# Kernel optimization log

Hardware: AMD Instinct MI355X
Metric: run time of the kernel (lower is better)

The kernel has to match this reference:

```python
import jax, jax.numpy as jnp
import numpy as np

NUM_HEADS = 128
QK_NOPE = 128
QK_ROPE = 64
V_HEAD = 128
Q_HEAD_DIM = 192
SOFTMAX_SCALE = 1.0 / np.sqrt(192.0)


def _rope_interleave(x, cos, sin):
    # x: [b,h,s,d]; reorder interleaved pairs to half-split layout then rotate
    b, h, s, d = x.shape
    x = x.reshape(b, h, s, d // 2, 2).swapaxes(3, 4).reshape(b, h, s, d)
    x1, x2 = x[..., : d // 2], x[..., d // 2:]
    rot = jnp.concatenate([-x2, x1], axis=-1)
    return x * cos + rot * sin


def setup_inputs() -> dict:
    key = jax.random.key(0)
    ks = jax.random.split(key, 8)
    bsz, q_len = 16, 1
    q_lora, kv_lora = 1536, 512
    cache_cap = 4096
    start_pos = 2048
    s = 0.05
    q_normed_dn = jax.random.normal(ks[0], (bsz, q_len, q_lora), jnp.float32) * s
    compressed_kv = jax.random.normal(ks[1], (bsz, q_len, kv_lora), jnp.float32) * s
    k_pe = jax.random.normal(ks[2], (bsz, 1, q_len, QK_ROPE), jnp.float32) * s
    position_ids = jnp.full((bsz, q_len), start_pos, dtype=jnp.int64)
    ckv_cache = jax.random.normal(ks[3], (bsz, cache_cap, kv_lora), jnp.float32) * s
    k_pe_cache = jax.random.normal(ks[4], (bsz, cache_cap, QK_ROPE), jnp.float32) * s
    # rope caches over full positions
    pos = jnp.arange(cache_cap, dtype=jnp.float32)
    inv = 1.0 / (10000.0 ** (jnp.arange(0, QK_ROPE, 2, dtype=jnp.float32) / QK_ROPE))
    freqs = pos[:, None] * inv[None, :]
    emb = jnp.concatenate([freqs, freqs], axis=-1)
    sin_cache = jnp.sin(emb)
    cos_cache = jnp.cos(emb)
    wkv_b = jax.random.normal(ks[5], (NUM_HEADS, QK_NOPE + V_HEAD, kv_lora), jnp.float32) * s
    wq_b = jax.random.normal(ks[6], (NUM_HEADS * Q_HEAD_DIM, q_lora), jnp.float32) * s
    return {
        "q_normed_dn": q_normed_dn,
        "compressed_kv": compressed_kv,
        "k_pe": k_pe,
        "position_ids": position_ids,
        "start_pos": start_pos,
        "ckv_cache": ckv_cache,
        "k_pe_cache": k_pe_cache,
        "sin_cache": sin_cache,
        "cos_cache": cos_cache,
        "wkv_b": wkv_b,
        "wq_b": wq_b,
    }


def reference(q_normed_dn, compressed_kv, k_pe, position_ids, start_pos,
              ckv_cache, k_pe_cache, sin_cache, cos_cache, wkv_b, wq_b):
    bsz, q_len, q_lora = q_normed_dn.shape
    kv_lora = compressed_kv.shape[-1]

    # split absorbed query projection
    wq_b_t = wq_b.T.reshape(q_lora, NUM_HEADS, Q_HEAD_DIM)  # [l,h,192]
    q_nope = jnp.einsum('bsl,lhd->bhsd', q_normed_dn, wq_b_t[:, :, :QK_NOPE])
    q_pe = jnp.einsum('bsl,lhd->bhsd', q_normed_dn, wq_b_t[:, :, QK_NOPE:])

    # matrix absorption: q_nope projected into latent space via w_ukv
    w_ukv = wkv_b[:, :QK_NOPE]                         # [h,128,c]
    q_nope = jnp.einsum('bshd,hdc->bshc', q_nope.swapaxes(1, 2), w_ukv)  # [b,s,h,c]

    # RoPE on q_pe and k_pe using gathered cos/sin at position_ids
    cos = cos_cache[position_ids][:, None]   # [b,1,s,d]
    sin = sin_cache[position_ids][:, None]
    q_pe = _rope_interleave(q_pe, cos, sin)            # [b,h,s,64]
    k_pe = _rope_interleave(k_pe, cos, sin)            # [b,1,s,64]
    q_pe = q_pe.swapaxes(1, 2)                         # [b,s,h,64]
    k_pe = k_pe[:, 0]                                  # [b,s,64]

    # append new tokens to caches at start_pos (q_len new tokens)
    ckv_cache = jax.lax.dynamic_update_slice(ckv_cache, compressed_kv, (0, start_pos, 0))
    k_pe_cache = jax.lax.dynamic_update_slice(k_pe_cache, k_pe, (0, start_pos, 0))
    kv_len = start_pos + q_len
    ckv = ckv_cache[:, :kv_len]                        # [b,n,c]
    kpe = k_pe_cache[:, :kv_len]                       # [b,n,64]

    # MLA decode attention in latent space (q_len==1, causal trivially satisfied)
    # scores = q_nope . ckv + q_pe . kpe
    scores = (jnp.einsum('bshc,bnc->bhsn', q_nope, ckv) +
              jnp.einsum('bshd,bnd->bhsn', q_pe, kpe)) * SOFTMAX_SCALE
    probs = jax.nn.softmax(scores, axis=-1)
    o = jnp.einsum('bhsn,bnc->bshc', probs, ckv)       # [b,s,h,c]
    o = o.reshape(bsz * q_len, NUM_HEADS, kv_lora)

    # project latent output to v_head_dim via tail of wkv_b
    attn_output = jnp.einsum('bhc,hdc->bhd', o, wkv_b[:, -V_HEAD:])
    return attn_output
```

## Files before the change

kernel.cpp:

```cpp
#include <hip/hip_runtime.h>
#include <hip/hip_bf16.h>
#include <math.h>

typedef __attribute__((ext_vector_type(8))) short short8x;
typedef __attribute__((ext_vector_type(4))) float f32x4;
typedef __attribute__((ext_vector_type(4))) unsigned short u16x4;
typedef __attribute__((ext_vector_type(8))) unsigned short u16x8;

#define NSPLIT 16
#define NTILE 66
#define KVROWS (NTILE * 32)

__device__ __forceinline__ unsigned short f2bf(float x) {
  unsigned int u = __float_as_uint(x);
  u += 0x7fffu + ((u >> 16) & 1u);
  return (unsigned short)(u >> 16);
}
__device__ __forceinline__ float bf2f(unsigned short u) {
  return __uint_as_float(((unsigned int)u) << 16);
}
__device__ __forceinline__ u16x4 cvt4(float4 v) {
  u16x4 r;
  r[0] = f2bf(v.x); r[1] = f2bf(v.y); r[2] = f2bf(v.z); r[3] = f2bf(v.w);
  return r;
}
__device__ __forceinline__ void gload_lds16(const void* g, void* l) {
  __builtin_amdgcn_global_load_lds(
      (const __attribute__((address_space(1))) unsigned int*)g,
      (__attribute__((address_space(3))) unsigned int*)l, 16, 0, 0);
}

__global__ __launch_bounds__(256) void kA(
    const float* __restrict__ ckvc, const float* __restrict__ kpec,
    const float* __restrict__ ckvn, const float* __restrict__ kpein,
    const float* __restrict__ cosc, const float* __restrict__ sinc,
    const int* __restrict__ sposp, int cap,
    unsigned short* __restrict__ kvbf,
    const float* __restrict__ wq, const float* __restrict__ x,
    float* __restrict__ qfull) {
  const int bx = blockIdx.x;
  const int tid = threadIdx.x;

  if (bx < 384) {
    const int lane = tid & 63, wid = tid >> 6;
    const int l15 = lane & 15, lg = lane >> 4;
    const int rowb = bx * 64 + wid * 16;
    const float* wrow = wq + (size_t)(rowb + l15) * 1536 + lg * 8;
    const float* xrow = x + l15 * 1536 + lg * 8;

    f32x4 aHH = (f32x4){0.f, 0.f, 0.f, 0.f};
    f32x4 aHL = (f32x4){0.f, 0.f, 0.f, 0.f};
    f32x4 aLH = (f32x4){0.f, 0.f, 0.f, 0.f};
    f32x4 bHH = (f32x4){0.f, 0.f, 0.f, 0.f};
    f32x4 bHL = (f32x4){0.f, 0.f, 0.f, 0.f};
    f32x4 bLH = (f32x4){0.f, 0.f, 0.f, 0.f};
#pragma unroll 8
    for (int kc = 0; kc < 48; ++kc) {
      const float4 wA = *(const float4*)(wrow + kc * 32);
      const float4 wB = *(const float4*)(wrow + kc * 32 + 4);
      const float4 xA = *(const float4*)(xrow + kc * 32);
      const float4 xB = *(const float4*)(xrow + kc * 32 + 4);
      const float wf[8] = {wA.x, wA.y, wA.z, wA.w, wB.x, wB.y, wB.z, wB.w};
      const float xf[8] = {xA.x, xA.y, xA.z, xA.w, xB.x, xB.y, xB.z, xB.w};
      short8x ah, al, bh, bl;
#pragma unroll
      for (int e = 0; e < 8; ++e) {
        const unsigned int wu = __float_as_uint(wf[e]);
        const float whf = __uint_as_float(wu & 0xffff0000u);
        ah[e] = (short)(wu >> 16);
        al[e] = (short)(__float_as_uint(wf[e] - whf) >> 16);
        const unsigned int xu = __float_as_uint(xf[e]);
        const float xhf = __uint_as_float(xu & 0xffff0000u);
        bh[e] = (short)(xu >> 16);
        bl[e] = (short)(__float_as_uint(xf[e] - xhf) >> 16);
      }
      if (kc & 1) {
        bHH = __builtin_amdgcn_mfma_f32_16x16x32_bf16(ah, bh, bHH, 0, 0, 0);
        bHL = __builtin_amdgcn_mfma_f32_16x16x32_bf16(ah, bl, bHL, 0, 0, 0);
        bLH = __builtin_amdgcn_mfma_f32_16x16x32_bf16(al, bh, bLH, 0, 0, 0);
      } else {
        aHH = __builtin_amdgcn_mfma_f32_16x16x32_bf16(ah, bh, aHH, 0, 0, 0);
        aHL = __builtin_amdgcn_mfma_f32_16x16x32_bf16(ah, bl, aHL, 0, 0, 0);
        aLH = __builtin_amdgcn_mfma_f32_16x16x32_bf16(al, bh, aLH, 0, 0, 0);
      }
    }
    const f32x4 acc = (aHH + bHH) + (aHL + bHL) + (aLH + bLH);
#pragma unroll
    for (int r = 0; r < 4; ++r)
      qfull[(size_t)l15 * 24576 + rowb + lg * 4 + r] = acc[r];
  } else {
    const int bxx = bx - 384;
    const int spos = sposp[0];
#pragma unroll
    for (int i = 0; i < 8; ++i) {
      const int u = bxx * 2048 + i * 256 + tid;
      const int b = u / 304128;
      const int r = u - b * 304128;
      const int n = r / 144;
      const int c4 = (r - n * 144) * 4;
      float4 v = make_float4(0.f, 0.f, 0.f, 0.f);
      if (n < spos) {
        if (c4 < 512) v = *(const float4*)(ckvc + ((size_t)b * cap + n) * 512 + c4);
        else          v = *(const float4*)(kpec + ((size_t)b * cap + n) * 64 + (c4 - 512));
      } else if (n == spos) {
        if (c4 < 512) v = *(const float4*)(ckvn + (size_t)b * 512 + c4);
        else {
          const int d = c4 - 512;
          const float* kp = kpein + b * 64;
          float o[4];
          if (d < 32) {
#pragma unroll
            for (int k = 0; k < 4; ++k) {
              int j = d + k;
              o[k] = kp[2 * j] * cosc[spos * 64 + j] - kp[2 * j + 1] * sinc[spos * 64 + j];
            }
          } else {
#pragma unroll
            for (int k = 0; k < 4; ++k) {
              int j = d - 32 + k;
              o[k] = kp[2 * j + 1] * cosc[spos * 64 + j] + kp[2 * j] * sinc[spos * 64 + j];
            }
          }
          v = make_float4(o[0], o[1], o[2], o[3]);
        }
      }
      *(u16x4*)(kvbf + (size_t)u * 4) = cvt4(v);
    }
  }
}

__global__ __launch_bounds__(256) void kB2(
    const float* __restrict__ qfull, const float* __restrict__ wkv,
    const float* __restrict__ cosc, const float* __restrict__ sinc,
    const int* __restrict__ sposp, unsigned short* __restrict__ qcat,
    const unsigned short* __restrict__ kvbf, unsigned short* __restrict__ vT) {
  __shared__ __align__(16) unsigned char shbuf[36864];
  const int bx = blockIdx.x;
  const int tid = threadIdx.x;

  if (bx < 256) {
    float* qs = (float*)shbuf;
    const int h = bx & 127;
    const int half = bx >> 7;
    for (int u = tid; u < 2048; u += 256) {
      int bb = u >> 7, d = u & 127;
      qs[u] = qfull[bb * 24576 + h * 192 + d];
    }
    __syncthreads();
    const int c = half * 256 + tid;
    float acc[16];
#pragma unroll
    for (int bb = 0; bb < 16; ++bb) acc[bb] = 0.f;
    const float* wbase = wkv + (size_t)h * 256 * 512;
    for (int d = 0; d < 128; ++d) {
      const float w = wbase[d * 512 + c];
#pragma unroll
      for (int bb = 0; bb < 16; ++bb) acc[bb] += qs[bb * 128 + d] * w;
    }
#pragma unroll
    for (int bb = 0; bb < 16; ++bb)
      qcat[(size_t)(bb * 128 + h) * 576 + c] = f2bf(acc[bb]);
  } else if (bx < 272) {
    const int b = bx - 256;
    const int pos = sposp[0];
#pragma unroll
    for (int i = 0; i < 16; ++i) {
      int idx = tid + i * 256;
      int h = idx >> 5, j = idx & 31;
      const float cj = cosc[pos * 64 + j];
      const float sj = sinc[pos * 64 + j];
      const float* src = qfull + b * 24576 + h * 192 + 128;
      float x0 = src[2 * j], x1 = src[2 * j + 1];
      unsigned short* dst = qcat + (size_t)(b * 128 + h) * 576 + 512;
      dst[j] = f2bf(x0 * cj - x1 * sj);
      dst[j + 32] = f2bf(x1 * cj + x0 * sj);
    }
  } else {
    unsigned short* tile_sh = (unsigned short*)shbuf;
    const int v_ = bx - 272;
    const int b = v_ / NTILE;
    const int tile = v_ - b * NTILE;
    const int wid = tid >> 6;
    const unsigned short* src = kvbf + ((size_t)b * KVROWS + tile * 32) * 576;
#pragma unroll
    for (int i = 0; i < 9; ++i) {
      const int ch = i * 256 + tid;
      const int row = ch / 72, cc = ch - row * 72;
      gload_lds16(src + row * 576 + ((cc ^ (row & 7)) * 8),
                  &tile_sh[(i * 256 + wid * 64) * 8]);
    }
    __syncthreads();
    unsigned short* vdst = vT + ((size_t)b * NTILE + tile) * 18432;
#pragma unroll
    for (int r = 0; r < 9; ++r) {
      const int c = r * 64 + (tid >> 2);
      const int q = tid & 3;
      const int c8 = c >> 3, c7 = c & 7;
      u16x8 w;
#pragma unroll
      for (int j = 0; j < 8; ++j)
        w[j] = tile_sh[(q * 8 + j) * 576 + ((c8 ^ j) << 3) + c7];
      *(u16x8*)(vdst + c * 32 + q * 8) = w;
    }
  }
}

__global__ __launch_bounds__(512, 2) void k4_attn(
    const unsigned short* __restrict__ kvbf, const unsigned short* __restrict__ vT,
    const unsigned short* __restrict__ qcat, const int* __restrict__ sposp,
    unsigned short* __restrict__ opart, float* __restrict__ mlp) {
  __shared__ __align__(16) unsigned short kv_sh[2][32 * 576];
  __shared__ __align__(16) unsigned short vt_sh[2][512 * 32];
  __shared__ __align__(16) unsigned short p_sh[8 * 640];

  const int tid = threadIdx.x;
  const int split = blockIdx.x, b = blockIdx.y;
  const int kvlen = sposp[0] + 1;
  const int lane = tid & 63, wid = tid >> 6;
  const int l15 = lane & 15, lg = lane >> 4;

  const unsigned short* kvb = kvbf + (size_t)b * KVROWS * 576;
  const unsigned short* vtb = vT + (size_t)b * NTILE * 18432;

  const int vro = lane >> 2, vq = lane & 3;
  const int vgq = vq ^ ((vro >> 1) & 3);

  auto STAGE = [&](int pb, int tt) {
    const unsigned short* ksrc = kvb + (size_t)tt * 32 * 576;
    for (int j = wid; j < 36; j += 8) {
      int u = j * 64 + lane;
      int row = u / 72, cc = u - row * 72;
      gload_lds16(ksrc + row * 576 + ((cc ^ (row & 7)) * 8), &kv_sh[pb][j * 512]);
    }
    const unsigned short* vsrc = vtb + (size_t)tt * 18432;
    for (int j = wid; j < 32; j += 8)
      gload_lds16(vsrc + j * 512 + vro * 32 + vgq * 8, &vt_sh[pb][j * 512]);
  };

  STAGE(0, split);

  const int hrow = b * 128 + wid * 16 + l15;
  const unsigned short* qrow = qcat + (size_t)hrow * 576;
  short8x qf[18];
#pragma unroll
  for (int s = 0; s < 18; ++s)
    qf[s] = *(const short8x*)(qrow + s * 32 + lg * 8);

  f32x4 acc[32];
#pragma unroll
  for (int i = 0; i < 32; ++i) acc[i] = (f32x4){0.f, 0.f, 0.f, 0.f};
  float mold[4] = {-1e30f, -1e30f, -1e30f, -1e30f};
  float lsum[4] = {0.f, 0.f, 0.f, 0.f};
  const float C2 = (1.0f / sqrtf(192.0f)) * 1.4426950408889634f;

  const int vrd = ((lg ^ ((l15 >> 1) & 3)) << 3);

  int pb = 0;
  for (int tt = split; tt * 32 < kvlen; tt += NSPLIT, pb ^= 1) {
    __syncthreads();
    if ((tt + NSPLIT) * 32 < kvlen) STAGE(pb ^ 1, tt + NSPLIT);
    const int n0 = tt * 32;

    f32x4 D0 = (f32x4){0.f, 0.f, 0.f, 0.f};
    f32x4 D1 = (f32x4){0.f, 0.f, 0.f, 0.f};
#pragma unroll
    for (int s = 0; s < 18; ++s) {
      const int c8 = (s * 4 + lg) ^ (l15 & 7);
      short8x fb0 = *(const short8x*)&kv_sh[pb][l15 * 576 + c8 * 8];
      short8x fb1 = *(const short8x*)&kv_sh[pb][(16 + l15) * 576 + c8 * 8];
      D0 = __builtin_amdgcn_mfma_f32_16x16x32_bf16(qf[s], fb0, D0, 0, 0, 0);
      D1 = __builtin_amdgcn_mfma_f32_16x16x32_bf16(qf[s], fb1, D1, 0, 0, 0);
    }

    const bool v0 = (n0 + l15) < kvlen;
    const bool v1 = (n0 + 16 + l15) < kvlen;
    float alpha[4];
#pragma unroll
    for (int r = 0; r < 4; ++r) {
      const float t0 = v0 ? D0[r] * C2 : -1e30f;
      const float t1 = v1 ? D1[r] * C2 : -1e30f;
      float mx = fmaxf(t0, t1);
      mx = fmaxf(mx, __shfl_xor(mx, 1, 64));
      mx = fmaxf(mx, __shfl_xor(mx, 2, 64));
      mx = fmaxf(mx, __shfl_xor(mx, 4, 64));
      mx = fmaxf(mx, __shfl_xor(mx, 8, 64));
      const float mn = fmaxf(mold[r], mx);
      alpha[r] = exp2f(mold[r] - mn);
      const float p0 = v0 ? exp2f(t0 - mn) : 0.f;
      const float p1 = v1 ? exp2f(t1 - mn) : 0.f;
      float rs = p0 + p1;
      rs += __shfl_xor(rs, 1, 64);
      rs += __shfl_xor(rs, 2, 64);
      rs += __shfl_xor(rs, 4, 64);
      rs += __shfl_xor(rs, 8, 64);
      lsum[r] = lsum[r] * alpha[r] + rs;
      mold[r] = mn;
      p_sh[wid * 640 + (lg * 4 + r) * 40 + l15] = f2bf(p0);
      p_sh[wid * 640 + (lg * 4 + r) * 40 + 16 + l15] = f2bf(p1);
    }
    const f32x4 av = {alpha[0], alpha[1], alpha[2], alpha[3]};
#pragma unroll
    for (int cg = 0; cg < 32; ++cg) acc[cg] *= av;

    const short8x pa = *(const short8x*)&p_sh[wid * 640 + l15 * 40 + lg * 8];
#pragma unroll
    for (int cg = 0; cg < 32; ++cg) {
      short8x bv = *(const short8x*)&vt_sh[pb][cg * 512 + l15 * 32 + vrd];
      acc[cg] = __builtin_amdgcn_mfma_f32_16x16x32_bf16(pa, bv, acc[cg], 0, 0, 0);
    }
  }

  const int hbm_ = b * 128 + wid * 16 + lg * 4;
  if (l15 == 0) {
#pragma unroll
    for (int r = 0; r < 4; ++r) {
      mlp[(size_t)(hbm_ + r) * (2 * NSPLIT) + split * 2] = mold[r];
      mlp[(size_t)(hbm_ + r) * (2 * NSPLIT) + split * 2 + 1] = lsum[r];
    }
  }

  __syncthreads();
  unsigned short* ep = &kv_sh[0][0] + wid * 8192;
#pragma unroll
  for (int cg = 0; cg < 32; ++cg)
#pragma unroll
    for (int r = 0; r < 4; ++r)
      ep[(lg * 4 + r) * 512 + cg * 16 + l15] = f2bf(acc[cg][r]);
#pragma unroll
  for (int r16 = 0; r16 < 16; ++r16) {
    const int bh = b * 128 + wid * 16 + r16;
    const size_t ob = ((size_t)bh * NSPLIT + split) * 512;
#pragma unroll
    for (int i = 0; i < 2; ++i)
      *(u16x4*)&opart[ob + i * 256 + lane * 4] =
          *(const u16x4*)&ep[r16 * 512 + i * 256 + lane * 4];
  }
}

__global__ __launch_bounds__(512) void kC_out(
    const unsigned short* __restrict__ opart, const float* __restrict__ mlp,
    const float* __restrict__ wkv, float* __restrict__ out) {
  __shared__ float os[16 * 512];
  __shared__ float wsc[16 * 16];
  __shared__ float lsc[16];
  const int h = blockIdx.x;
  const int tid = threadIdx.x;

  if (tid < 16) {
    const int b = tid;
    const float* m = mlp + (size_t)(b * 128 + h) * (2 * NSPLIT);
    float mi[NSPLIT], li[NSPLIT], M = -1e30f;
#pragma unroll
    for (int i = 0; i < NSPLIT; ++i) {
      mi[i] = m[i * 2];
      li[i] = m[i * 2 + 1];
      M = fmaxf(M, mi[i]);
    }
    float Ls = 0.f;
#pragma unroll
    for (int i = 0; i < NSPLIT; ++i) {
      const float w = exp2f(mi[i] - M);
      Ls += li[i] * w;
      wsc[b * NSPLIT + i] = w;
    }
    lsc[b] = Ls;
  }
  __syncthreads();

  for (int u = tid; u < 8192; u += 512) {
    const int b = u >> 9, c = u & 511;
    const unsigned short* op = opart + (size_t)(b * 128 + h) * NSPLIT * 512 + c;
    float o = 0.f;
#pragma unroll
    for (int i = 0; i < NSPLIT; ++i) o += wsc[b * NSPLIT + i] * bf2f(op[i * 512]);
    os[u] = o / lsc[b];
  }
  __syncthreads();

  const int d = tid >> 2, cq = tid & 3;
  const float* wrow = wkv + ((size_t)(h * 256 + 128 + d)) * 512;
  float acc[16];
#pragma unroll
  for (int bb = 0; bb < 16; ++bb) acc[bb] = 0.f;
  for (int i = 0; i < 32; ++i) {
    const int c = cq * 4 + i * 16;
    const float4 w4 = *(const float4*)&wrow[c];
#pragma unroll
    for (int bb = 0; bb < 16; ++bb) {
      const float4 o4 = *(const float4*)&os[bb * 512 + c];
      acc[bb] += w4.x * o4.x + w4.y * o4.y + w4.z * o4.z + w4.w * o4.w;
    }
  }
#pragma unroll
  for (int bb = 0; bb < 16; ++bb) {
    float v = acc[bb];
    v += __shfl_xor(v, 1, 64);
    v += __shfl_xor(v, 2, 64);
    if (cq == 0) out[(size_t)(bb * 128 + h) * 128 + d] = v;
  }
}

extern "C" void kernel_launch(void* const* d_in, const int* in_sizes, int n_in,
                              void* d_out, int out_size, void* d_ws, size_t ws_size,
                              hipStream_t stream) {
  const float* x = (const float*)d_in[0];
  const float* ckvn = (const float*)d_in[1];
  const float* kpein = (const float*)d_in[2];
  const int* sposp = (const int*)d_in[4];
  const float* ckvc = (const float*)d_in[5];
  const float* kpec = (const float*)d_in[6];
  const float* sinc = (const float*)d_in[7];
  const float* cosc = (const float*)d_in[8];
  const float* wkv = (const float*)d_in[9];
  const float* wq = (const float*)d_in[10];
  float* out = (float*)d_out;

  const int cap = in_sizes[5] / (16 * 512);

  float* ws = (float*)d_ws;
  float* qfull = ws;
  float* mlp = ws + 393216;
  unsigned short* qcat = (unsigned short*)(ws + 458752);
  unsigned short* kvbf = (unsigned short*)(ws + 1048576);
  unsigned short* vT   = (unsigned short*)(ws + 10780672);
  unsigned short* opart = (unsigned short*)(ws + 20512768);

  kA<<<dim3(384 + 2376), 256, 0, stream>>>(ckvc, kpec, ckvn, kpein, cosc, sinc,
                                           sposp, cap, kvbf, wq, x, qfull);
  kB2<<<dim3(272 + NTILE * 16), 256, 0, stream>>>(qfull, wkv, cosc, sinc, sposp,
                                                  qcat, kvbf, vT);
  k4_attn<<<dim3(NSPLIT, 16), 512, 0, stream>>>(kvbf, vT, qcat, sposp, opart, mlp);
  kC_out<<<dim3(128), 512, 0, stream>>>(opart, mlp, wkv, out);
}
```

Measured before the change: 177.2 us.

## Split q-projection into separate LDS-staged split-K GEMM kernel with more blocks

Separates the fused kernel into two launches: a cache-packing kernel that converts the KV cache to bf16, and a new q-projection GEMM kernel. The new GEMM stages 8 weight rows per block into swizzled LDS via direct global-to-LDS loads. It splits the K dimension across the 4 waves and reduces the partial sums through LDS, which lifts the grid from 384 to 3072 blocks. The aim is better bandwidth and occupancy on the large wq read, at the cost of an extra kernel launch, wasted MFMA columns (only 8 of 16 rows are used), and losing the overlap that came from running both tasks in one launch.

```diff
diff --git a/kernel.cpp b/kernel.cpp
--- a/kernel.cpp
+++ b/kernel.cpp
@@ -30,102 +30,127 @@
       (__attribute__((address_space(3))) unsigned int*)l, 16, 0, 0);
 }
 
-__global__ __launch_bounds__(256) void kA(
+__global__ __launch_bounds__(256, 3) void k1q(
+    const float* __restrict__ wq, const float* __restrict__ x,
+    float* __restrict__ qfull) {
+  __shared__ __align__(16) float wlds[8 * 1536];
+  const int bx = blockIdx.x;
+  const int tid = threadIdx.x;
+  const int lane = tid & 63, wid = tid >> 6;
+  const int l15 = lane & 15, lg = lane >> 4;
+
+  const float* wqb = wq + (size_t)bx * 8 * 1536;
+#pragma unroll
+  for (int i = 0; i < 12; ++i) {
+    const int u = i * 256 + tid;
+    const int row = u / 384;
+    const int cw = u - row * 384;
+    gload_lds16(wqb + ((size_t)row * 384 + (cw ^ (row & 7))) * 4, &wlds[u * 4]);
+  }
+
+  const int arow = l15 & 7;
+  const float* xrow = x + (size_t)l15 * 1536 + wid * 384 + lg * 8;
+
+  f32x4 aHH = (f32x4){0.f, 0.f, 0.f, 0.f};
+  f32x4 aHL = (f32x4){0.f, 0.f, 0.f, 0.f};
+  f32x4 aLH = (f32x4){0.f, 0.f, 0.f, 0.f};
+  f32x4 bHH = (f32x4){0.f, 0.f, 0.f, 0.f};
+  f32x4 bHL = (f32x4){0.f, 0.f, 0.f, 0.f};
+  f32x4 bLH = (f32x4){0.f, 0.f, 0.f, 0.f};
+
+  __syncthreads();
+
+#pragma unroll
+  for (int kc = 0; kc < 12; ++kc) {
+    const int cw0 = wid * 96 + kc * 8 + lg * 2;
+    const float4 wA = *(const float4*)&wlds[((size_t)arow * 384 + (cw0 ^ arow)) * 4];
+    const float4 wB = *(const float4*)&wlds[((size_t)arow * 384 + ((cw0 + 1) ^ arow)) * 4];
+    const float4 xA = *(const float4*)(xrow + kc * 32);
+    const float4 xB = *(const float4*)(xrow + kc * 32 + 4);
+    const float wf[8] = {wA.x, wA.y, wA.z, wA.w, wB.x, wB.y, wB.z, wB.w};
+    const float xf[8] = {xA.x, xA.y, xA.z, xA.w, xB.x, xB.y, xB.z, xB.w};
+    short8x ah, al, bh, bl;
+#pragma unroll
+    for (int e = 0; e < 8; ++e) {
+      const unsigned int wu = __float_as_uint(wf[e]);
+      const float whf = __uint_as_float(wu & 0xffff0000u);
+      ah[e] = (short)(wu >> 16);
+      al[e] = (short)(__float_as_uint(wf[e] - whf) >> 16);
+      const unsigned int xu = __float_as_uint(xf[e]);
+      const float xhf = __uint_as_float(xu & 0xffff0000u);
+      bh[e] = (short)(xu >> 16);
+      bl[e] = (short)(__float_as_uint(xf[e] - xhf) >> 16);
+    }
+    if (kc & 1) {
+      bHH = __builtin_amdgcn_mfma_f32_16x16x32_bf16(ah, bh, bHH, 0, 0, 0);
+      bHL = __builtin_amdgcn_mfma_f32_16x16x32_bf16(ah, bl, bHL, 0, 0, 0);
+      bLH = __builtin_amdgcn_mfma_f32_16x16x32_bf16(al, bh, bLH, 0, 0, 0);
+    } else {
+      aHH = __builtin_amdgcn_mfma_f32_16x16x32_bf16(ah, bh, aHH, 0, 0, 0);
+      aHL = __builtin_amdgcn_mfma_f32_16x16x32_bf16(ah, bl, aHL, 0, 0, 0);
+      aLH = __builtin_amdgcn_mfma_f32_16x16x32_bf16(al, bh, aLH, 0, 0, 0);
+    }
+  }
+  f32x4 acc = (aHH + bHH) + (aHL + bHL) + (aLH + bLH);
+
+  __syncthreads();
+  if (wid != 0) *(f32x4*)&wlds[wid * 256 + lane * 4] = acc;
+  __syncthreads();
+  if (wid == 0) {
+    acc += *(const f32x4*)&wlds[256 + lane * 4];
+    acc += *(const f32x4*)&wlds[512 + lane * 4];
+    acc += *(const f32x4*)&wlds[768 + lane * 4];
+    if (lg < 2) {
+#pragma unroll
+      for (int r = 0; r < 4; ++r)
+        qfull[(size_t)l15 * 24576 + bx * 8 + lg * 4 + r] = acc[r];
+    }
+  }
+}
+
+__global__ __launch_bounds__(256) void kPA(
     const float* __restrict__ ckvc, const float* __restrict__ kpec,
     const float* __restrict__ ckvn, const float* __restrict__ kpein,
     const float* __restrict__ cosc, const float* __restrict__ sinc,
     const int* __restrict__ sposp, int cap,
-    unsigned short* __restrict__ kvbf,
-    const float* __restrict__ wq, const float* __restrict__ x,
-    float* __restrict__ qfull) {
-  const int bx = blockIdx.x;
+    unsigned short* __restrict__ kvbf) {
+  const int bxx = blockIdx.x;
   const int tid = threadIdx.x;
-
-  if (bx < 384) {
-    const int lane = tid & 63, wid = tid >> 6;
-    const int l15 = lane & 15, lg = lane >> 4;
-    const int rowb = bx * 64 + wid * 16;
-    const float* wrow = wq + (size_t)(rowb + l15) * 1536 + lg * 8;
-    const float* xrow = x + l15 * 1536 + lg * 8;
-
-    f32x4 aHH = (f32x4){0.f, 0.f, 0.f, 0.f};
-    f32x4 aHL = (f32x4){0.f, 0.f, 0.f, 0.f};
-    f32x4 aLH = (f32x4){0.f, 0.f, 0.f, 0.f};
-    f32x4 bHH = (f32x4){0.f, 0.f, 0.f, 0.f};
-    f32x4 bHL = (f32x4){0.f, 0.f, 0.f, 0.f};
-    f32x4 bLH = (f32x4){0.f, 0.f, 0.f, 0.f};
-#pragma unroll 8
-    for (int kc = 0; kc < 48; ++kc) {
-      const float4 wA = *(const float4*)(wrow + kc * 32);
-      const float4 wB = *(const float4*)(wrow + kc * 32 + 4);
-      const float4 xA = *(const float4*)(xrow + kc * 32);
-      const float4 xB = *(const float4*)(xrow + kc * 32 + 4);
-      const float wf[8] = {wA.x, wA.y, wA.z, wA.w, wB.x, wB.y, wB.z, wB.w};
-      const float xf[8] = {xA.x, xA.y, xA.z, xA.w, xB.x, xB.y, xB.z, xB.w};
-      short8x ah, al, bh, bl;
-#pragma unroll
-      for (int e = 0; e < 8; ++e) {
-        const unsigned int wu = __float_as_uint(wf[e]);
-        const float whf = __uint_as_float(wu & 0xffff0000u);
-        ah[e] = (short)(wu >> 16);
-        al[e] = (short)(__float_as_uint(wf[e] - whf) >> 16);
-        const unsigned int xu = __float_as_uint(xf[e]);
-        const float xhf = __uint_as_float(xu & 0xffff0000u);
-        bh[e] = (short)(xu >> 16);
-        bl[e] = (short)(__float_as_uint(xf[e] - xhf) >> 16);
+  const int spos = sposp[0];
+#pragma unroll
+  for (int i = 0; i < 8; ++i) {
+    const int u = bxx * 2048 + i * 256 + tid;
+    const int b = u / 304128;
+    const int r = u - b * 304128;
+    const int n = r / 144;
+    const int c4 = (r - n * 144) * 4;
+    float4 v = make_float4(0.f, 0.f, 0.f, 0.f);
+    if (n < spos) {
+      if (c4 < 512) v = *(const float4*)(ckvc + ((size_t)b * cap + n) * 512 + c4);
+      else          v = *(const float4*)(kpec + ((size_t)b * cap + n) * 64 + (c4 - 512));
+    } else if (n == spos) {
+      if (c4 < 512) v = *(const float4*)(ckvn + (size_t)b * 512 + c4);
+      else {
+        const int d = c4 - 512;
+        const float* kp = kpein + b * 64;
+        float o[4];
+        if (d < 32) {
+#pragma unroll
+          for (int k = 0; k < 4; ++k) {
+            int j = d + k;
+            o[k] = kp[2 * j] * cosc[spos * 64 + j] - kp[2 * j + 1] * sinc[spos * 64 + j];
+          }
+        } else {
+#pragma unroll
+          for (int k = 0; k < 4; ++k) {
+            int j = d - 32 + k;
+            o[k] = kp[2 * j + 1] * cosc[spos * 64 + j] + kp[2 * j] * sinc[spos * 64 + j];
+          }
+        }
+        v = make_float4(o[0], o[1], o[2], o[3]);
       }
-      if (kc & 1) {
-        bHH = __builtin_amdgcn_mfma_f32_16x16x32_bf16(ah, bh, bHH, 0, 0, 0);
-        bHL = __builtin_amdgcn_mfma_f32_16x16x32_bf16(ah, bl, bHL, 0, 0, 0);
-        bLH = __builtin_amdgcn_mfma_f32_16x16x32_bf16(al, bh, bLH, 0, 0, 0);
-      } else {
-        aHH = __builtin_amdgcn_mfma_f32_16x16x32_bf16(ah, bh, aHH, 0, 0, 0);
-        aHL = __builtin_amdgcn_mfma_f32_16x16x32_bf16(ah, bl, aHL, 0, 0, 0);
-        aLH = __builtin_amdgcn_mfma_f32_16x16x32_bf16(al, bh, aLH, 0, 0, 0);
-      }
-    }
-    const f32x4 acc = (aHH + bHH) + (aHL + bHL) + (aLH + bLH);
-#pragma unroll
-    for (int r = 0; r < 4; ++r)
-      qfull[(size_t)l15 * 24576 + rowb + lg * 4 + r] = acc[r];
-  } else {
-    const int bxx = bx - 384;
-    const int spos = sposp[0];
-#pragma unroll
-    for (int i = 0; i < 8; ++i) {
-      const int u = bxx * 2048 + i * 256 + tid;
-      const int b = u / 304128;
-      const int r = u - b * 304128;
-      const int n = r / 144;
-      const int c4 = (r - n * 144) * 4;
-      float4 v = make_float4(0.f, 0.f, 0.f, 0.f);
-      if (n < spos) {
-        if (c4 < 512) v = *(const float4*)(ckvc + ((size_t)b * cap + n) * 512 + c4);
-        else          v = *(const float4*)(kpec + ((size_t)b * cap + n) * 64 + (c4 - 512));
-      } else if (n == spos) {
-        if (c4 < 512) v = *(const float4*)(ckvn + (size_t)b * 512 + c4);
-        else {
-          const int d = c4 - 512;
-          const float* kp = kpein + b * 64;
-          float o[4];
-          if (d < 32) {
-#pragma unroll
-            for (int k = 0; k < 4; ++k) {
-              int j = d + k;
-              o[k] = kp[2 * j] * cosc[spos * 64 + j] - kp[2 * j + 1] * sinc[spos * 64 + j];
-            }
-          } else {
-#pragma unroll
-            for (int k = 0; k < 4; ++k) {
-              int j = d - 32 + k;
-              o[k] = kp[2 * j + 1] * cosc[spos * 64 + j] + kp[2 * j] * sinc[spos * 64 + j];
-            }
-          }
-          v = make_float4(o[0], o[1], o[2], o[3]);
-        }
-      }
-      *(u16x4*)(kvbf + (size_t)u * 4) = cvt4(v);
-    }
+    }
+    *(u16x4*)(kvbf + (size_t)u * 4) = cvt4(v);
   }
 }
 
@@ -144,7 +169,7 @@
     const int half = bx >> 7;
     for (int u = tid; u < 2048; u += 256) {
       int bb = u >> 7, d = u & 127;
-      qs[u] = qfull[bb * 24576 + h * 192 + d];
+      qs[u] = qfull[(size_t)bb * 24576 + h * 192 + d];
     }
     __syncthreads();
     const int c = half * 256 + tid;
@@ -169,7 +194,7 @@
       int h = idx >> 5, j = idx & 31;
       const float cj = cosc[pos * 64 + j];
       const float sj = sinc[pos * 64 + j];
-      const float* src = qfull + b * 24576 + h * 192 + 128;
+      const float* src = qfull + (size_t)b * 24576 + h * 192 + 128;
       float x0 = src[2 * j], x1 = src[2 * j + 1];
       unsigned short* dst = qcat + (size_t)(b * 128 + h) * 576 + 512;
       dst[j] = f2bf(x0 * cj - x1 * sj);
@@ -425,8 +450,9 @@
   unsigned short* vT   = (unsigned short*)(ws + 10780672);
   unsigned short* opart = (unsigned short*)(ws + 20512768);
 
-  kA<<<dim3(384 + 2376), 256, 0, stream>>>(ckvc, kpec, ckvn, kpein, cosc, sinc,
-                                           sposp, cap, kvbf, wq, x, qfull);
+  kPA<<<dim3(2376), 256, 0, stream>>>(ckvc, kpec, ckvn, kpein, cosc, sinc,
+                                      sposp, cap, kvbf);
+  k1q<<<dim3(3072), 256, 0, stream>>>(wq, x, qfull);
   kB2<<<dim3(272 + NTILE * 16), 256, 0, stream>>>(qfull, wkv, cosc, sinc, sposp,
                                                   qcat, kvbf, vT);
   k4_attn<<<dim3(NSPLIT, 16), 512, 0, stream>>>(kvbf, vT, qcat, sposp, opart, mlp);
```

Result: slower. 190.9 us (+7.7%).
